# Performance work log

Hardware: AMD Instinct MI355X
Metric: run time of the kernel (lower is better)

Reference implementation:

```python
import jax, jax.numpy as jnp
import numpy as np

NUM_HEADS = 8
SPLIT = 2  # split_size; idx=0 -> H_sp=H, W_sp=SPLIT (horizontal stripes)


def setup_inputs() -> dict:
    key = jax.random.key(0)
    k1, k2, k3 = jax.random.split(key, 3)
    B, C, H, W = 4, 64, 128, 128
    temp = jax.random.normal(k1, (B, 3, C, H, W), dtype=jnp.float32)
    conv_w = jax.random.normal(k2, (C, 1, 3, 3), dtype=jnp.float32) * 0.1  # depthwise OIHW
    conv_b = jax.random.normal(k3, (C,), dtype=jnp.float32) * 0.1
    return {"temp": temp, "conv_w": conv_w, "conv_b": conv_b}


def reference(temp, conv_w, conv_b):
    B, _, C, H, W = temp.shape
    hd = C // NUM_HEADS
    scale = hd ** (-0.5)
    H_sp, W_sp = H, SPLIT  # idx == 0

    # symmetric pad to multiples of window size (faithful to original; zero here)
    H_pad = (H_sp - H % H_sp) % H_sp
    W_pad = (W_sp - W % W_sp) % W_sp
    top, left = H_pad // 2, W_pad // 2
    x = jnp.pad(temp, ((0, 0), (0, 0), (0, 0), (top, H_pad - top), (left, W_pad - left)))
    H_, W_ = H + H_pad, W + W_pad
    q, k, v = x[:, 0], x[:, 1], x[:, 2]  # each [B,C,H_,W_]

    nW = (H_ // H_sp) * (W_ // W_sp)
    N = H_sp * W_sp  # tokens per window

    def im2cswin(t):
        # [B,C,H_,W_] -> [B*nW, heads, N, hd]
        w = t.reshape(B, C, H_ // H_sp, H_sp, W_ // W_sp, W_sp)
        w = w.transpose(0, 2, 4, 3, 5, 1).reshape(-1, N, C)
        return w.reshape(-1, N, NUM_HEADS, hd).transpose(0, 2, 1, 3)

    qh = im2cswin(q) * scale
    kh = im2cswin(k)

    # v windows as images [B*nW, C, H_sp, W_sp] for depthwise LePE conv
    vw = v.reshape(B, C, H_ // H_sp, H_sp, W_ // W_sp, W_sp)
    vw = vw.transpose(0, 2, 4, 1, 3, 5).reshape(-1, C, H_sp, W_sp)
    rpe = jax.lax.conv_general_dilated(
        vw, conv_w, window_strides=(1, 1), padding='SAME',
        feature_group_count=C, dimension_numbers=('NCHW', 'OIHW', 'NCHW'))
    rpe = rpe + conv_b[None, :, None, None]

    vh = vw.reshape(-1, NUM_HEADS, hd, N).transpose(0, 1, 3, 2)    # [B*nW,h,N,hd]
    rpeh = rpe.reshape(-1, NUM_HEADS, hd, N).transpose(0, 1, 3, 2)

    attn = jax.nn.softmax(jnp.einsum('whnd,whmd->whnm', qh, kh), axis=-1)
    out = jnp.einsum('whnm,whmd->whnd', attn, vh) + rpeh           # [B*nW,h,N,hd]

    out = out.transpose(0, 2, 1, 3).reshape(-1, N, C)              # [B*nW,N,C]
    # windows2img + crop
    out = out.reshape(B, H_ // H_sp, W_ // W_sp, H_sp, W_sp, C)
    out = out.transpose(0, 1, 3, 2, 4, 5).reshape(B, H_, W_, C)
    out = out[:, top:H + top, left:W + left, :]
    return out.reshape(B, H * W, C)
```

## Files before the change

kernel.cpp:

```cpp
#include <hip/hip_runtime.h>
#include <hip/hip_bf16.h>
#include <stdint.h>


typedef __attribute__((ext_vector_type(4))) short bf16x4;
typedef __attribute__((ext_vector_type(4))) float f32x4;

static __device__ __forceinline__ uint32_t pk2(float x, float y) {
    union { __hip_bfloat162 h2; uint32_t u; } c;
    c.h2 = __float22bfloat162_rn(make_float2(x, y));
    return c.u;
}
static __device__ __forceinline__ float bflo(uint32_t u){ return __uint_as_float(u<<16); }
static __device__ __forceinline__ float bfhi(uint32_t u){ return __uint_as_float(u & 0xffff0000u); }

static __device__ __forceinline__ uint2 ld2(const char* p) {
    uint2 r;
    r.x = *(const uint32_t*)(p);
    r.y = *(const uint32_t*)(p + 4);
    return r;
}

static __device__ __forceinline__ int qk_off(int tok) {
    return (tok * 16) ^ ((tok >> 4 & 7) << 4);
}

static __device__ __forceinline__ f32x4 mfma16x16x16bf16(bf16x4 a, bf16x4 b, f32x4 c) {
#if __has_builtin(__builtin_amdgcn_mfma_f32_16x16x16bf16_1k)
    return __builtin_amdgcn_mfma_f32_16x16x16bf16_1k(a, b, c, 0, 0, 0);
#else
    f32x4 d;
    asm volatile("v_mfma_f32_16x16x16_bf16 %0, %1, %2, %3\n\ts_nop 7\n\ts_nop 7"
                 : "=v"(d) : "v"(a), "v"(b), "v"(c));
    return d;
#endif
}

#define QK_WIN_STR 4128
#define V_CH_STR   536
#define V_WIN_STR  4288

__global__ __launch_bounds__(512, 4)
void lepe_attn(const float* __restrict__ temp,
               const float* __restrict__ conv_w,
               const float* __restrict__ conv_b,
               float* __restrict__ out)
{
    __shared__ __align__(16) char smem[50496];
    char* q_s = smem;
    char* k_s = smem + 16512;
    char* v_t = smem + 33024;
    float* cw_s = (float*)(smem + 50176);

    const int tid  = threadIdx.x;
    const int wave = tid >> 6, lane = tid & 63;
    const int lr = lane & 15, quad = lane >> 4;
    const int win   = wave & 3;
    const int qbase = (wave >> 2) * 8;

    const int bid = blockIdx.x;
    const int x  = bid & 7;
    int t_ = bid >> 3;
    const int wjh  = t_ & 1;  t_ >>= 1;
    const int head = t_ & 7;
    const int b    = t_ >> 3;
    const int wi   = x*8 + wjh*4 + win;

    const size_t cstr = 16384, sstr = 64 * cstr;
    const float qs = 0.35355339059327373f * 1.4426950408889634f;

    {
        const int cg = wave;
        const int hg = lane >> 1, hf1 = lane & 1;
        const int w0 = hf1 * 2;
        const float* bp = temp + (size_t)b*3*sstr + (size_t)(head*8 + cg)*cstr
                        + x*16 + wjh*8 + hf1*4;
        #pragma unroll
        for (int i = 0; i < 4; ++i) {
            int h = i*32 + hg;
            int o0 = qk_off(2*h), o1 = qk_off(2*h + 1);
            float4 fq = *(const float4*)(bp + (size_t)h*128);
            uint32_t a0 = pk2(fq.x*qs, fq.y*qs);
            uint32_t a1 = pk2(fq.z*qs, fq.w*qs);
            *(uint16_t*)(q_s + w0*QK_WIN_STR     + o0 + cg*2) = (uint16_t)a0;
            *(uint16_t*)(q_s + w0*QK_WIN_STR     + o1 + cg*2) = (uint16_t)(a0>>16);
            *(uint16_t*)(q_s + (w0+1)*QK_WIN_STR + o0 + cg*2) = (uint16_t)a1;
            *(uint16_t*)(q_s + (w0+1)*QK_WIN_STR + o1 + cg*2) = (uint16_t)(a1>>16);
            float4 fk = *(const float4*)(bp + sstr + (size_t)h*128);
            uint32_t b0 = pk2(fk.x, fk.y);
            uint32_t b1 = pk2(fk.z, fk.w);
            *(uint16_t*)(k_s + w0*QK_WIN_STR     + o0 + cg*2) = (uint16_t)b0;
            *(uint16_t*)(k_s + w0*QK_WIN_STR     + o1 + cg*2) = (uint16_t)(b0>>16);
            *(uint16_t*)(k_s + (w0+1)*QK_WIN_STR + o0 + cg*2) = (uint16_t)b1;
            *(uint16_t*)(k_s + (w0+1)*QK_WIN_STR + o1 + cg*2) = (uint16_t)(b1>>16);
            float4 fv = *(const float4*)(bp + 2*sstr + (size_t)h*128);
            *(uint32_t*)(v_t + w0*V_WIN_STR     + cg*V_CH_STR + 4*h + 4) = pk2(fv.x, fv.y);
            *(uint32_t*)(v_t + (w0+1)*V_WIN_STR + cg*V_CH_STR + 4*h + 4) = pk2(fv.z, fv.w);
        }
        if (tid < 72) cw_s[tid] = conv_w[head*72 + tid];
        if (tid < 8)  cw_s[72 + tid] = conv_b[head*8 + tid];
        if (tid < 32) {
            int vw = tid >> 3, vc = tid & 7;
            *(uint32_t*)(v_t + vw*V_WIN_STR + vc*V_CH_STR)       = 0;
            *(uint32_t*)(v_t + vw*V_WIN_STR + vc*V_CH_STR + 516) = 0;
        }
    }
    __syncthreads();

    const f32x4 zf = {0.f, 0.f, 0.f, 0.f};
    const uint2 z2 = make_uint2(0, 0);
    const uint2 ones2 = make_uint2(0x3F803F80u, 0x3F803F80u);
    uint2 kf[16]; uint2 vf[16];
    #pragma unroll
    for (int T = 0; T < 16; ++T) {
        uint2 kk = ld2(k_s + win*QK_WIN_STR + qk_off(T*16 + lr) + (quad & 1)*8);
        kf[T] = (quad < 2) ? kk : z2;
        uint2 vv = ld2(v_t + win*V_WIN_STR + (lane & 7)*V_CH_STR + 4 + (T*16 + quad*4)*2);
        vf[T] = (lr < 8) ? vv : ((lr == 8) ? ones2 : z2);
    }
    __syncthreads();

    {
        const int w2  = tid >> 7;
        const int chl = (tid >> 4) & 7;
        const int seg = tid & 15;
        const char* base = v_t + w2*V_WIN_STR + chl*V_CH_STR + seg*32;
        uint32_t d[10];
        *(uint2*)(d+0) = *(const uint2*)(base);
        *(uint2*)(d+2) = *(const uint2*)(base+8);
        *(uint2*)(d+4) = *(const uint2*)(base+16);
        *(uint2*)(d+6) = *(const uint2*)(base+24);
        *(uint2*)(d+8) = *(const uint2*)(base+32);
        float w9[9];
        #pragma unroll
        for (int k = 0; k < 9; ++k) w9[k] = cw_s[chl*9 + k];
        const float bia = cw_s[72 + chl];
        #pragma unroll
        for (int tt = 0; tt < 16; ++tt) {
            int tok = seg*16 + tt;
            int w01 = tok & 1;
            int L = (tt >> 1) * 2;
            float rp = bia;
            #pragma unroll
            for (int dy = 0; dy < 3; ++dy) {
                #pragma unroll
                for (int wp = 0; wp < 2; ++wp) {
                    int idx = L + 2*dy + wp;
                    uint32_t dw = d[idx >> 1];
                    float tap = (idx & 1) ? bfhi(dw) : bflo(dw);
                    rp = fmaf(w9[dy*3 + wp + 1 - w01], tap, rp);
                }
            }
            union { __hip_bfloat16 h; uint16_t u; } cv;
            cv.h = __float2bfloat16(rp);
            *(uint16_t*)(k_s + w2*QK_WIN_STR + qk_off(tok) + chl*2) = cv.u;
        }
    }
    __syncthreads();

    #pragma unroll 1
    for (int qg0 = 0; qg0 < 8; ++qg0) {
        const int qg = qbase + qg0;
        uint2 qq = ld2(q_s + win*QK_WIN_STR + qk_off(qg*16 + lr) + (quad & 1)*8);
        union { uint2 u; bf16x4 h4; } qf; qf.u = (quad < 2) ? qq : z2;
        f32x4 acc0 = zf, acc1 = zf;
        #pragma unroll
        for (int T = 0; T < 16; T += 2) {
            union { uint2 u; bf16x4 h4; } kfu0; kfu0.u = kf[T];
            union { uint2 u; bf16x4 h4; } kfu1; kfu1.u = kf[T+1];
            f32x4 sc0 = mfma16x16x16bf16(kfu0.h4, qf.h4, zf);
            f32x4 sc1 = mfma16x16x16bf16(kfu1.h4, qf.h4, zf);
            float a0 = __builtin_amdgcn_exp2f(sc0[0]);
            float a1 = __builtin_amdgcn_exp2f(sc0[1]);
            float a2 = __builtin_amdgcn_exp2f(sc0[2]);
            float a3 = __builtin_amdgcn_exp2f(sc0[3]);
            float b0_ = __builtin_amdgcn_exp2f(sc1[0]);
            float b1_ = __builtin_amdgcn_exp2f(sc1[1]);
            float b2_ = __builtin_amdgcn_exp2f(sc1[2]);
            float b3_ = __builtin_amdgcn_exp2f(sc1[3]);
            union { uint2 u; bf16x4 h4; } pb0; pb0.u = make_uint2(pk2(a0,a1), pk2(a2,a3));
            union { uint2 u; bf16x4 h4; } pb1; pb1.u = make_uint2(pk2(b0_,b1_), pk2(b2_,b3_));
            union { uint2 u; bf16x4 h4; } vf0; vf0.u = vf[T];
            union { uint2 u; bf16x4 h4; } vf1; vf1.u = vf[T+1];
            acc0 = mfma16x16x16bf16(vf0.h4, pb0.h4, acc0);
            acc1 = mfma16x16x16bf16(vf1.h4, pb1.h4, acc1);
        }
        f32x4 acc;
        acc[0] = acc0[0] + acc1[0];
        acc[1] = acc0[1] + acc1[1];
        acc[2] = acc0[2] + acc1[2];
        acc[3] = acc0[3] + acc1[3];
        float rs = __shfl(acc[0], 32 + lr);
        const float rinv = __builtin_amdgcn_rcpf(rs);
        if (quad < 2) {
            int tok = qg*16 + lr;
            int h = tok >> 1, w01 = tok & 1;
            uint2 rp2 = ld2(k_s + win*QK_WIN_STR + qk_off(tok) + quad*8);
            float4 ov;
            ov.x = fmaf(acc[0], rinv, bflo(rp2.x));
            ov.y = fmaf(acc[1], rinv, bfhi(rp2.x));
            ov.z = fmaf(acc[2], rinv, bflo(rp2.y));
            ov.w = fmaf(acc[3], rinv, bfhi(rp2.y));
            size_t addr = (size_t)b*1048576 + (size_t)(h*128 + wi*2 + w01)*64
                        + head*8 + quad*4;
            *(float4*)(out + addr) = ov;
        }
    }
}

extern "C" void kernel_launch(void* const* d_in, const int* in_sizes, int n_in,
                              void* d_out, int out_size, void* d_ws, size_t ws_size,
                              hipStream_t stream) {
    const float* temp = (const float*)d_in[0];
    const float* cw   = (const float*)d_in[1];
    const float* cb   = (const float*)d_in[2];
    float* o = (float*)d_out;
    (void)in_sizes; (void)n_in; (void)out_size; (void)d_ws; (void)ws_size;
    lepe_attn<<<dim3(512), dim3(512), 0, stream>>>(temp, cw, cb, o);
}
```

Measured before the change: 116.1 us.

## Halve block size to two windows per block and double grid

Each block now handles 2 stripe windows with 4 waves (256 threads) instead of 4 windows with 8 waves, and the grid is doubled to 1024 blocks. Shared memory per block is halved and the global load mapping is rewritten so each thread loads one float4 of a channel row for two adjacent windows. The goal is better load balance and occupancy across the 256 CUs, since 512 blocks underfilled the machine. In exchange, each load moves only 16 contiguous bytes per row and there are more blocks to schedule.

```diff
diff --git a/kernel.cpp b/kernel.cpp
--- a/kernel.cpp
+++ b/kernel.cpp
@@ -40,66 +40,65 @@
 #define V_CH_STR   536
 #define V_WIN_STR  4288
 
-__global__ __launch_bounds__(512, 4)
+__global__ __launch_bounds__(256, 4)
 void lepe_attn(const float* __restrict__ temp,
                const float* __restrict__ conv_w,
                const float* __restrict__ conv_b,
                float* __restrict__ out)
 {
-    __shared__ __align__(16) char smem[50496];
+    __shared__ __align__(16) char smem[25408];
     char* q_s = smem;
-    char* k_s = smem + 16512;
-    char* v_t = smem + 33024;
-    float* cw_s = (float*)(smem + 50176);
+    char* k_s = smem + 8256;
+    char* v_t = smem + 16512;
+    float* cw_s = (float*)(smem + 25088);
 
     const int tid  = threadIdx.x;
     const int wave = tid >> 6, lane = tid & 63;
     const int lr = lane & 15, quad = lane >> 4;
-    const int win   = wave & 3;
-    const int qbase = (wave >> 2) * 8;
+    const int win   = wave & 1;
+    const int qbase = (wave >> 1) * 8;
 
     const int bid = blockIdx.x;
     const int x  = bid & 7;
     int t_ = bid >> 3;
-    const int wjh  = t_ & 1;  t_ >>= 1;
+    const int wq   = t_ & 3;  t_ >>= 2;
     const int head = t_ & 7;
     const int b    = t_ >> 3;
-    const int wi   = x*8 + wjh*4 + win;
+    const int wi   = x*8 + wq*2 + win;
 
     const size_t cstr = 16384, sstr = 64 * cstr;
     const float qs = 0.35355339059327373f * 1.4426950408889634f;
 
     {
-        const int cg = wave;
-        const int hg = lane >> 1, hf1 = lane & 1;
-        const int w0 = hf1 * 2;
-        const float* bp = temp + (size_t)b*3*sstr + (size_t)(head*8 + cg)*cstr
-                        + x*16 + wjh*8 + hf1*4;
         #pragma unroll
         for (int i = 0; i < 4; ++i) {
-            int h = i*32 + hg;
+            int r  = i*256 + tid;
+            int ch = r >> 7;
+            int h  = r & 127;
+            const float* bp = temp + (size_t)b*3*sstr + (size_t)(head*8 + ch)*cstr
+                            + (size_t)h*128 + x*16 + wq*4;
             int o0 = qk_off(2*h), o1 = qk_off(2*h + 1);
-            float4 fq = *(const float4*)(bp + (size_t)h*128);
+            float4 fq = *(const float4*)(bp);
             uint32_t a0 = pk2(fq.x*qs, fq.y*qs);
             uint32_t a1 = pk2(fq.z*qs, fq.w*qs);
-            *(uint16_t*)(q_s + w0*QK_WIN_STR     + o0 + cg*2) = (uint16_t)a0;
-            *(uint16_t*)(q_s + w0*QK_WIN_STR     + o1 + cg*2) = (uint16_t)(a0>>16);
-            *(uint16_t*)(q_s + (w0+1)*QK_WIN_STR + o0 + cg*2) = (uint16_t)a1;
-            *(uint16_t*)(q_s + (w0+1)*QK_WIN_STR + o1 + cg*2) = (uint16_t)(a1>>16);
-            float4 fk = *(const float4*)(bp + sstr + (size_t)h*128);
+            *(uint16_t*)(q_s + o0 + ch*2)              = (uint16_t)a0;
+            *(uint16_t*)(q_s + o1 + ch*2)              = (uint16_t)(a0>>16);
+            *(uint16_t*)(q_s + QK_WIN_STR + o0 + ch*2) = (uint16_t)a1;
+            *(uint16_t*)(q_s + QK_WIN_STR + o1 + ch*2) = (uint16_t)(a1>>16);
+            float4 fk = *(const float4*)(bp + sstr);
             uint32_t b0 = pk2(fk.x, fk.y);
             uint32_t b1 = pk2(fk.z, fk.w);
-            *(uint16_t*)(k_s + w0*QK_WIN_STR     + o0 + cg*2) = (uint16_t)b0;
-            *(uint16_t*)(k_s + w0*QK_WIN_STR     + o1 + cg*2) = (uint16_t)(b0>>16);
-            *(uint16_t*)(k_s + (w0+1)*QK_WIN_STR + o0 + cg*2) = (uint16_t)b1;
-            *(uint16_t*)(k_s + (w0+1)*QK_WIN_STR + o1 + cg*2) = (uint16_t)(b1>>16);
-            float4 fv = *(const float4*)(bp + 2*sstr + (size_t)h*128);
-            *(uint32_t*)(v_t + w0*V_WIN_STR     + cg*V_CH_STR + 4*h + 4) = pk2(fv.x, fv.y);
-            *(uint32_t*)(v_t + (w0+1)*V_WIN_STR + cg*V_CH_STR + 4*h + 4) = pk2(fv.z, fv.w);
+            *(uint16_t*)(k_s + o0 + ch*2)              = (uint16_t)b0;
+            *(uint16_t*)(k_s + o1 + ch*2)              = (uint16_t)(b0>>16);
+            *(uint16_t*)(k_s + QK_WIN_STR + o0 + ch*2) = (uint16_t)b1;
+            *(uint16_t*)(k_s + QK_WIN_STR + o1 + ch*2) = (uint16_t)(b1>>16);
+            float4 fv = *(const float4*)(bp + 2*sstr);
+            *(uint32_t*)(v_t + ch*V_CH_STR + 4*h + 4)             = pk2(fv.x, fv.y);
+            *(uint32_t*)(v_t + V_WIN_STR + ch*V_CH_STR + 4*h + 4) = pk2(fv.z, fv.w);
         }
         if (tid < 72) cw_s[tid] = conv_w[head*72 + tid];
         if (tid < 8)  cw_s[72 + tid] = conv_b[head*8 + tid];
-        if (tid < 32) {
+        if (tid < 16) {
             int vw = tid >> 3, vc = tid & 7;
             *(uint32_t*)(v_t + vw*V_WIN_STR + vc*V_CH_STR)       = 0;
             *(uint32_t*)(v_t + vw*V_WIN_STR + vc*V_CH_STR + 516) = 0;
@@ -216,5 +215,5 @@
     const float* cb   = (const float*)d_in[2];
     float* o = (float*)d_out;
     (void)in_sizes; (void)n_in; (void)out_size; (void)d_ws; (void)ws_size;
-    lepe_attn<<<dim3(512), dim3(512), 0, stream>>>(temp, cw, cb, o);
-}
+    lepe_attn<<<dim3(1024), dim3(256), 0, stream>>>(temp, cw, cb, o);
+}
```

New measurement: 112.8 us. 2.9% less time.

## Restructure LePE conv per row pair and prefetch next Q/rpe fragments

Applied to the files above, without the earlier changes.

The depthwise conv now assigns each thread one row (two tokens) across all 8 channels. It reuses the loaded taps for both the even and odd outputs and writes full 16-byte rows into the k_s buffer, instead of many scattered 2-byte stores. Conv weights are padded to a stride of 12 so they can be read as vectors. In the attention loop the next Q and rpe fragments are loaded one iteration ahead, and the wave priority is raised around the MFMA/exp block. Shared memory grows slightly, and the prefetch adds register pressure.

```diff
diff --git a/kernel.cpp b/kernel.cpp
--- a/kernel.cpp
+++ b/kernel.cpp
@@ -46,7 +46,7 @@
                const float* __restrict__ conv_b,
                float* __restrict__ out)
 {
-    __shared__ __align__(16) char smem[50496];
+    __shared__ __align__(16) char smem[50608];
     char* q_s = smem;
     char* k_s = smem + 16512;
     char* v_t = smem + 33024;
@@ -97,8 +97,11 @@
             *(uint32_t*)(v_t + w0*V_WIN_STR     + cg*V_CH_STR + 4*h + 4) = pk2(fv.x, fv.y);
             *(uint32_t*)(v_t + (w0+1)*V_WIN_STR + cg*V_CH_STR + 4*h + 4) = pk2(fv.z, fv.w);
         }
-        if (tid < 72) cw_s[tid] = conv_w[head*72 + tid];
-        if (tid < 8)  cw_s[72 + tid] = conv_b[head*8 + tid];
+        if (tid < 96) {
+            int ch = tid / 12, j = tid - ch*12;
+            cw_s[tid] = (j < 9) ? conv_w[head*72 + ch*9 + j] : 0.f;
+        }
+        if (tid < 8)  cw_s[96 + tid] = conv_b[head*8 + tid];
         if (tid < 32) {
             int vw = tid >> 3, vc = tid & 7;
             *(uint32_t*)(v_t + vw*V_WIN_STR + vc*V_CH_STR)       = 0;
@@ -121,49 +124,55 @@
     __syncthreads();
 
     {
-        const int w2  = tid >> 7;
-        const int chl = (tid >> 4) & 7;
-        const int seg = tid & 15;
-        const char* base = v_t + w2*V_WIN_STR + chl*V_CH_STR + seg*32;
-        uint32_t d[10];
-        *(uint2*)(d+0) = *(const uint2*)(base);
-        *(uint2*)(d+2) = *(const uint2*)(base+8);
-        *(uint2*)(d+4) = *(const uint2*)(base+16);
-        *(uint2*)(d+6) = *(const uint2*)(base+24);
-        *(uint2*)(d+8) = *(const uint2*)(base+32);
-        float w9[9];
+        const int w2 = tid >> 7;
+        const int p  = tid & 127;
+        const char* vb = v_t + w2*V_WIN_STR + 4*p;
+        float re[8], ro[8];
         #pragma unroll
-        for (int k = 0; k < 9; ++k) w9[k] = cw_s[chl*9 + k];
-        const float bia = cw_s[72 + chl];
-        #pragma unroll
-        for (int tt = 0; tt < 16; ++tt) {
-            int tok = seg*16 + tt;
-            int w01 = tok & 1;
-            int L = (tt >> 1) * 2;
-            float rp = bia;
-            #pragma unroll
-            for (int dy = 0; dy < 3; ++dy) {
-                #pragma unroll
-                for (int wp = 0; wp < 2; ++wp) {
-                    int idx = L + 2*dy + wp;
-                    uint32_t dw = d[idx >> 1];
-                    float tap = (idx & 1) ? bfhi(dw) : bflo(dw);
-                    rp = fmaf(w9[dy*3 + wp + 1 - w01], tap, rp);
-                }
-            }
-            union { __hip_bfloat16 h; uint16_t u; } cv;
-            cv.h = __float2bfloat16(rp);
-            *(uint16_t*)(k_s + w2*QK_WIN_STR + qk_off(tok) + chl*2) = cv.u;
-        }
+        for (int c = 0; c < 8; ++c) {
+            uint2 t01 = ld2(vb + c*V_CH_STR);
+            uint32_t t2 = *(const uint32_t*)(vb + c*V_CH_STR + 8);
+            float d0 = bflo(t01.x), d1 = bfhi(t01.x);
+            float d2 = bflo(t01.y), d3 = bfhi(t01.y);
+            float d4 = bflo(t2),    d5 = bfhi(t2);
+            float4 wA = *(const float4*)(cw_s + c*12);
+            float4 wB = *(const float4*)(cw_s + c*12 + 4);
+            float  w8 = cw_s[c*12 + 8];
+            float  bia = cw_s[96 + c];
+            float e = bia, o = bia;
+            e = fmaf(wA.y, d0, e); o = fmaf(wA.x, d0, o);
+            e = fmaf(wA.z, d1, e); o = fmaf(wA.y, d1, o);
+            e = fmaf(wB.x, d2, e); o = fmaf(wA.w, d2, o);
+            e = fmaf(wB.y, d3, e); o = fmaf(wB.x, d3, o);
+            e = fmaf(wB.w, d4, e); o = fmaf(wB.z, d4, o);
+            e = fmaf(w8,   d5, e); o = fmaf(wB.w, d5, o);
+            re[c] = e; ro[c] = o;
+        }
+        uint4 rowe = make_uint4(pk2(re[0],re[1]), pk2(re[2],re[3]),
+                                pk2(re[4],re[5]), pk2(re[6],re[7]));
+        uint4 rowo = make_uint4(pk2(ro[0],ro[1]), pk2(ro[2],ro[3]),
+                                pk2(ro[4],ro[5]), pk2(ro[6],ro[7]));
+        *(uint4*)(k_s + w2*QK_WIN_STR + qk_off(2*p))     = rowe;
+        *(uint4*)(k_s + w2*QK_WIN_STR + qk_off(2*p + 1)) = rowo;
     }
     __syncthreads();
 
+    const char* qwin = q_s + win*QK_WIN_STR;
+    const char* kwin = k_s + win*QK_WIN_STR;
+    const int tok0 = qbase*16 + lr;
+    uint2 qq = ld2(qwin + qk_off(tok0) + (quad & 1)*8);
+    uint2 rp = ld2(kwin + qk_off(tok0) + quad*8);
     #pragma unroll 1
     for (int qg0 = 0; qg0 < 8; ++qg0) {
-        const int qg = qbase + qg0;
-        uint2 qq = ld2(q_s + win*QK_WIN_STR + qk_off(qg*16 + lr) + (quad & 1)*8);
         union { uint2 u; bf16x4 h4; } qf; qf.u = (quad < 2) ? qq : z2;
+        const uint2 rpc = rp;
+        if (qg0 < 7) {
+            int tn = tok0 + (qg0 + 1)*16;
+            qq = ld2(qwin + qk_off(tn) + (quad & 1)*8);
+            rp = ld2(kwin + qk_off(tn) + quad*8);
+        }
         f32x4 acc0 = zf, acc1 = zf;
+        __builtin_amdgcn_s_setprio(1);
         #pragma unroll
         for (int T = 0; T < 16; T += 2) {
             union { uint2 u; bf16x4 h4; } kfu0; kfu0.u = kf[T];
@@ -185,6 +194,7 @@
             acc0 = mfma16x16x16bf16(vf0.h4, pb0.h4, acc0);
             acc1 = mfma16x16x16bf16(vf1.h4, pb1.h4, acc1);
         }
+        __builtin_amdgcn_s_setprio(0);
         f32x4 acc;
         acc[0] = acc0[0] + acc1[0];
         acc[1] = acc0[1] + acc1[1];
@@ -193,14 +203,13 @@
         float rs = __shfl(acc[0], 32 + lr);
         const float rinv = __builtin_amdgcn_rcpf(rs);
         if (quad < 2) {
-            int tok = qg*16 + lr;
+            int tok = (qbase + qg0)*16 + lr;
             int h = tok >> 1, w01 = tok & 1;
-            uint2 rp2 = ld2(k_s + win*QK_WIN_STR + qk_off(tok) + quad*8);
             float4 ov;
-            ov.x = fmaf(acc[0], rinv, bflo(rp2.x));
-            ov.y = fmaf(acc[1], rinv, bfhi(rp2.x));
-            ov.z = fmaf(acc[2], rinv, bflo(rp2.y));
-            ov.w = fmaf(acc[3], rinv, bfhi(rp2.y));
+            ov.x = fmaf(acc[0], rinv, bflo(rpc.x));
+            ov.y = fmaf(acc[1], rinv, bfhi(rpc.x));
+            ov.z = fmaf(acc[2], rinv, bflo(rpc.y));
+            ov.w = fmaf(acc[3], rinv, bfhi(rpc.y));
             size_t addr = (size_t)b*1048576 + (size_t)(h*128 + wi*2 + w01)*64
                         + head*8 + quad*4;
             *(float4*)(out + addr) = ov;
```

Measured after the change: 115.2 us. No clear change (-0.8%).

## Compute LePE conv in registers during load via wave shuffles, drop two barriers

Applied to the files above, without the earlier changes.

The depthwise 3x3 conv is now computed right after the V values are loaded, using cross-lane shuffles to fetch the neighbouring rows. Results go to a dedicated rpe shared buffer instead of overwriting k_s. This removes the separate conv phase, the re-reads of V from LDS and two __syncthreads. The cost is a larger shared allocation (about 66.7KB against about 50.5KB), which may cut occupancy below the 4 blocks per CU in launch_bounds, plus some extra register pressure.

```diff
diff --git a/kernel.cpp b/kernel.cpp
--- a/kernel.cpp
+++ b/kernel.cpp
@@ -46,11 +46,11 @@
                const float* __restrict__ conv_b,
                float* __restrict__ out)
 {
-    __shared__ __align__(16) char smem[50496];
-    char* q_s = smem;
-    char* k_s = smem + 16512;
-    char* v_t = smem + 33024;
-    float* cw_s = (float*)(smem + 50176);
+    __shared__ __align__(16) char smem[66688];
+    char* q_s   = smem;
+    char* k_s   = smem + 16512;
+    char* rpe_s = smem + 33024;
+    char* v_t   = smem + 49536;
 
     const int tid  = threadIdx.x;
     const int wave = tid >> 6, lane = tid & 63;
@@ -75,6 +75,7 @@
         const int w0 = hf1 * 2;
         const float* bp = temp + (size_t)b*3*sstr + (size_t)(head*8 + cg)*cstr
                         + x*16 + wjh*8 + hf1*4;
+        uint32_t p0[4], p1[4];
         #pragma unroll
         for (int i = 0; i < 4; ++i) {
             int h = i*32 + hg;
@@ -94,15 +95,46 @@
             *(uint16_t*)(k_s + (w0+1)*QK_WIN_STR + o0 + cg*2) = (uint16_t)b1;
             *(uint16_t*)(k_s + (w0+1)*QK_WIN_STR + o1 + cg*2) = (uint16_t)(b1>>16);
             float4 fv = *(const float4*)(bp + 2*sstr + (size_t)h*128);
-            *(uint32_t*)(v_t + w0*V_WIN_STR     + cg*V_CH_STR + 4*h + 4) = pk2(fv.x, fv.y);
-            *(uint32_t*)(v_t + (w0+1)*V_WIN_STR + cg*V_CH_STR + 4*h + 4) = pk2(fv.z, fv.w);
-        }
-        if (tid < 72) cw_s[tid] = conv_w[head*72 + tid];
-        if (tid < 8)  cw_s[72 + tid] = conv_b[head*8 + tid];
-        if (tid < 32) {
-            int vw = tid >> 3, vc = tid & 7;
-            *(uint32_t*)(v_t + vw*V_WIN_STR + vc*V_CH_STR)       = 0;
-            *(uint32_t*)(v_t + vw*V_WIN_STR + vc*V_CH_STR + 516) = 0;
+            p0[i] = pk2(fv.x, fv.y);
+            p1[i] = pk2(fv.z, fv.w);
+            *(uint32_t*)(v_t + w0*V_WIN_STR     + cg*V_CH_STR + 4*h + 4) = p0[i];
+            *(uint32_t*)(v_t + (w0+1)*V_WIN_STR + cg*V_CH_STR + 4*h + 4) = p1[i];
+        }
+        float w9[9];
+        #pragma unroll
+        for (int k = 0; k < 9; ++k) w9[k] = conv_w[head*72 + cg*9 + k];
+        const float bia = conv_b[head*8 + cg];
+        #pragma unroll
+        for (int wsel = 0; wsel < 2; ++wsel) {
+            const uint32_t* p = wsel ? p1 : p0;
+            char* rbase = rpe_s + (w0 + wsel)*QK_WIN_STR;
+            uint32_t dn[4], up[4];
+            #pragma unroll
+            for (int i = 0; i < 4; ++i) {
+                dn[i] = (uint32_t)__shfl((int)p[i], (lane - 2) & 63);
+                up[i] = (uint32_t)__shfl((int)p[i], (lane + 2) & 63);
+            }
+            #pragma unroll
+            for (int i = 0; i < 4; ++i) {
+                int h = i*32 + hg;
+                uint32_t pm  = (i > 0) ? dn[i-1] : 0u;
+                uint32_t nx_ = (i < 3) ? up[i+1] : 0u;
+                uint32_t prev = (lane < 2)  ? pm  : dn[i];
+                uint32_t next = (lane >= 62) ? nx_ : up[i];
+                float d0 = bflo(prev), d1 = bfhi(prev);
+                float d2 = bflo(p[i]), d3 = bfhi(p[i]);
+                float d4 = bflo(next), d5 = bfhi(next);
+                float e = bia, o = bia;
+                e = fmaf(w9[1], d0, e); o = fmaf(w9[0], d0, o);
+                e = fmaf(w9[2], d1, e); o = fmaf(w9[1], d1, o);
+                e = fmaf(w9[4], d2, e); o = fmaf(w9[3], d2, o);
+                e = fmaf(w9[5], d3, e); o = fmaf(w9[4], d3, o);
+                e = fmaf(w9[7], d4, e); o = fmaf(w9[6], d4, o);
+                e = fmaf(w9[8], d5, e); o = fmaf(w9[7], d5, o);
+                uint32_t eo = pk2(e, o);
+                *(uint16_t*)(rbase + qk_off(2*h)   + cg*2) = (uint16_t)eo;
+                *(uint16_t*)(rbase + qk_off(2*h+1) + cg*2) = (uint16_t)(eo >> 16);
+            }
         }
     }
     __syncthreads();
@@ -118,45 +150,6 @@
         uint2 vv = ld2(v_t + win*V_WIN_STR + (lane & 7)*V_CH_STR + 4 + (T*16 + quad*4)*2);
         vf[T] = (lr < 8) ? vv : ((lr == 8) ? ones2 : z2);
     }
-    __syncthreads();
-
-    {
-        const int w2  = tid >> 7;
-        const int chl = (tid >> 4) & 7;
-        const int seg = tid & 15;
-        const char* base = v_t + w2*V_WIN_STR + chl*V_CH_STR + seg*32;
-        uint32_t d[10];
-        *(uint2*)(d+0) = *(const uint2*)(base);
-        *(uint2*)(d+2) = *(const uint2*)(base+8);
-        *(uint2*)(d+4) = *(const uint2*)(base+16);
-        *(uint2*)(d+6) = *(const uint2*)(base+24);
-        *(uint2*)(d+8) = *(const uint2*)(base+32);
-        float w9[9];
-        #pragma unroll
-        for (int k = 0; k < 9; ++k) w9[k] = cw_s[chl*9 + k];
-        const float bia = cw_s[72 + chl];
-        #pragma unroll
-        for (int tt = 0; tt < 16; ++tt) {
-            int tok = seg*16 + tt;
-            int w01 = tok & 1;
-            int L = (tt >> 1) * 2;
-            float rp = bia;
-            #pragma unroll
-            for (int dy = 0; dy < 3; ++dy) {
-                #pragma unroll
-                for (int wp = 0; wp < 2; ++wp) {
-                    int idx = L + 2*dy + wp;
-                    uint32_t dw = d[idx >> 1];
-                    float tap = (idx & 1) ? bfhi(dw) : bflo(dw);
-                    rp = fmaf(w9[dy*3 + wp + 1 - w01], tap, rp);
-                }
-            }
-            union { __hip_bfloat16 h; uint16_t u; } cv;
-            cv.h = __float2bfloat16(rp);
-            *(uint16_t*)(k_s + w2*QK_WIN_STR + qk_off(tok) + chl*2) = cv.u;
-        }
-    }
-    __syncthreads();
 
     #pragma unroll 1
     for (int qg0 = 0; qg0 < 8; ++qg0) {
@@ -195,7 +188,7 @@
         if (quad < 2) {
             int tok = qg*16 + lr;
             int h = tok >> 1, w01 = tok & 1;
-            uint2 rp2 = ld2(k_s + win*QK_WIN_STR + qk_off(tok) + quad*8);
+            uint2 rp2 = ld2(rpe_s + win*QK_WIN_STR + qk_off(tok) + quad*8);
             float4 ov;
             ov.x = fmaf(acc[0], rinv, bflo(rp2.x));
             ov.y = fmaf(acc[1], rinv, bfhi(rp2.x));
```

New measurement: 115.7 us. About the same (-0.4%).
